# Kernel optimization log

Measured on AMD Instinct MI355X. Metric: run time of the kernel, lower is better.

Reference implementation:

```python
import jax, jax.numpy as jnp
import numpy as np

B, S, D, H, L, F = 1, 2048, 768, 12, 2, 3072
DH = D // H          # 64
W = 256              # one-sided sliding window (attention_window=512 total)
NC = S // W          # number of query chunks
VOCAB = 50265


def _ln(x, s, b, eps=1e-5):
    m = x.mean(-1, keepdims=True)
    v = ((x - m) ** 2).mean(-1, keepdims=True)
    return (x - m) / jnp.sqrt(v + eps) * s + b


def setup_inputs() -> dict:
    key = jax.random.key(0)
    ks = jax.random.split(key, 16)
    p = lambda k, sh: jax.random.normal(k, sh, jnp.float32) * 0.02
    return {
        "input_ids": jax.random.randint(ks[0], (B, S), 0, VOCAB),
        "attention_mask": jnp.ones((B, S), jnp.int32),
        "word_emb": p(ks[1], (VOCAB, D)),
        "pos_emb": p(ks[2], (S + 2, D)),          # roberta-style pos ids start at 2
        "type_emb": p(ks[3], (1, D)),
        "emb_ln_s": jnp.ones((D,), jnp.float32),
        "emb_ln_b": jnp.zeros((D,), jnp.float32),
        "Wqkv": p(ks[4], (L, 3, D, D)),
        "bqkv": jnp.zeros((L, 3, D), jnp.float32),
        "Wo": p(ks[5], (L, D, D)),
        "bo": jnp.zeros((L, D), jnp.float32),
        "ln1_s": jnp.ones((L, D), jnp.float32),
        "ln1_b": jnp.zeros((L, D), jnp.float32),
        "W1": p(ks[6], (L, D, F)),
        "b1": jnp.zeros((L, F), jnp.float32),
        "W2": p(ks[7], (L, F, D)),
        "b2": jnp.zeros((L, D), jnp.float32),
        "ln2_s": jnp.ones((L, D), jnp.float32),
        "ln2_b": jnp.zeros((L, D), jnp.float32),
        "pool_W": p(ks[8], (D, D)),
        "pool_b": jnp.zeros((D,), jnp.float32),
    }


def reference(input_ids, attention_mask, word_emb, pos_emb, type_emb,
              emb_ln_s, emb_ln_b, Wqkv, bqkv, Wo, bo, ln1_s, ln1_b,
              W1, b1, W2, b2, ln2_s, ln2_b, pool_W, pool_b):
    # ---- embeddings (roberta/longformer style) ----
    pos_ids = jnp.cumsum(attention_mask, axis=1) * attention_mask + 1  # padding_idx=1
    x = word_emb[input_ids] + pos_emb[pos_ids] + type_emb[0]
    x = _ln(x, emb_ln_s, emb_ln_b)

    # ---- banded-attention index/mask precompute (int constants) ----
    idx = jnp.arange(NC)[:, None] * W + jnp.arange(3 * W)[None, :]      # [NC, 3W] into padded seq
    rel = (jnp.arange(3 * W)[None, :] - W) - jnp.arange(W)[:, None]     # key_pos - query_pos
    band = (rel >= -W) & (rel <= W)                                      # [W, 3W]
    kmask = jnp.pad(attention_mask, ((0, 0), (W, W)))[:, idx].astype(bool)  # [B, NC, 3W]
    valid = band[None, None] & kmask[:, :, None, :]                      # [B, NC, W, 3W]

    inv_sqrt_dh = 1.0 / np.sqrt(DH)
    for l in range(L):
        qkv = jnp.einsum('bsd,tde->tbse', x, Wqkv[l]) + bqkv[l][:, None, None, :]
        q, k, v = [t.reshape(B, S, H, DH).transpose(0, 2, 1, 3) for t in qkv]  # [B,H,S,DH]
        qc = q.reshape(B, H, NC, W, DH)
        kp = jnp.pad(k, ((0, 0), (0, 0), (W, W), (0, 0)))
        vp = jnp.pad(v, ((0, 0), (0, 0), (W, W), (0, 0)))
        kc = kp[:, :, idx]                                               # [B,H,NC,3W,DH]
        vc = vp[:, :, idx]
        scores = jnp.einsum('bhcqd,bhckd->bhcqk', qc, kc) * inv_sqrt_dh  # [B,H,NC,W,3W]
        scores = jnp.where(valid[:, None], scores, -1e9)
        attn = jax.nn.softmax(scores, axis=-1)
        ctx = jnp.einsum('bhcqk,bhckd->bhcqd', attn, vc)
        ctx = ctx.reshape(B, H, S, DH).transpose(0, 2, 1, 3).reshape(B, S, D)
        x = _ln(x + ctx @ Wo[l] + bo[l], ln1_s[l], ln1_b[l])
        h = jax.nn.gelu(x @ W1[l] + b1[l], approximate=False)
        x = _ln(x + h @ W2[l] + b2[l], ln2_s[l], ln2_b[l])

    pooled = jnp.tanh(x[:, 0] @ pool_W + pool_b)
    return x, pooled
```

## Files before the change

### kernel.cpp

```cpp
#include <hip/hip_runtime.h>
#include <hip/hip_bf16.h>
#include <math.h>
#include <stddef.h>
#include <stdint.h>

typedef __hip_bfloat16 bf16;
typedef short bf16x8 __attribute__((ext_vector_type(8)));
typedef float f32x4 __attribute__((ext_vector_type(4)));

#define CS 2048
#define CD 768
#define CH 12
#define CDH 64
#define CF 3072
#define CW 256
#define CL 2
#define QKVN 2304
#define SDC ((size_t)CS * CD)

__device__ __forceinline__ void gload_lds16(const bf16* g, bf16* l) {
  __builtin_amdgcn_global_load_lds(
      (const __attribute__((address_space(1))) void*)g,
      (__attribute__((address_space(3))) void*)l, 16, 0, 0);
}

__device__ __forceinline__ float block_reduce_sum(float v, float* buf) {
  #pragma unroll
  for (int off = 32; off > 0; off >>= 1) v += __shfl_down(v, off, 64);
  int wid = threadIdx.x >> 6;
  __syncthreads();
  if ((threadIdx.x & 63) == 0) buf[wid] = v;
  __syncthreads();
  if (threadIdx.x == 0) buf[0] = buf[0] + buf[1] + buf[2] + buf[3];
  __syncthreads();
  return buf[0];
}

__global__ __launch_bounds__(256) void scan_kernel(const int* __restrict__ mask,
                                                   int* __restrict__ pos) {
  __shared__ int part[256];
  int tid = threadIdx.x;
  int mv[8]; int s = 0;
  #pragma unroll
  for (int i = 0; i < 8; ++i) { mv[i] = mask[tid * 8 + i]; s += mv[i]; }
  part[tid] = s;
  __syncthreads();
  for (int off = 1; off < 256; off <<= 1) {
    int t = 0;
    if (tid >= off) t = part[tid - off];
    __syncthreads();
    part[tid] += t;
    __syncthreads();
  }
  int run = part[tid] - s;
  #pragma unroll
  for (int i = 0; i < 8; ++i) {
    run += mv[i];
    pos[tid * 8 + i] = run * mv[i] + 1;
  }
}

__global__ __launch_bounds__(256) void transpose_conv(
    const float* __restrict__ in, bf16* __restrict__ out, int K, int N) {
  __shared__ float tile[32][33];
  int bn = blockIdx.x * 32, bk = blockIdx.y * 32;
  const float* src = in + (size_t)blockIdx.z * K * N;
  bf16* dst = out + (size_t)blockIdx.z * K * N;
  int tx = threadIdx.x, ty = threadIdx.y;
  #pragma unroll
  for (int i = 0; i < 32; i += 8)
    tile[ty + i][tx] = src[(size_t)(bk + ty + i) * N + bn + tx];
  __syncthreads();
  #pragma unroll
  for (int i = 0; i < 32; i += 8)
    dst[(size_t)(bn + ty + i) * K + bk + tx] = __float2bfloat16(tile[tx][ty + i]);
}

__global__ __launch_bounds__(256) void embed_ln_kernel(
    const int* __restrict__ ids, const int* __restrict__ pos,
    const float* __restrict__ wemb, const float* __restrict__ pemb,
    const float* __restrict__ temb, const float* __restrict__ gs,
    const float* __restrict__ gb, float* __restrict__ x, bf16* __restrict__ xb) {
  __shared__ float red[4];
  int srow = blockIdx.x;
  long long id = ids[srow];
  long long pid = pos[srow];
  float v[3];
  #pragma unroll
  for (int i = 0; i < 3; ++i) {
    int d = threadIdx.x + i * 256;
    v[i] = wemb[id * CD + d] + pemb[pid * CD + d] + temb[d];
  }
  float sum = v[0] + v[1] + v[2];
  sum = block_reduce_sum(sum, red);
  float mean = sum * (1.0f / CD);
  float sq = 0.f;
  #pragma unroll
  for (int i = 0; i < 3; ++i) { float c = v[i] - mean; sq += c * c; }
  sq = block_reduce_sum(sq, red);
  float rstd = rsqrtf(sq * (1.0f / CD) + 1e-5f);
  #pragma unroll
  for (int i = 0; i < 3; ++i) {
    int d = threadIdx.x + i * 256;
    float o = (v[i] - mean) * rstd * gs[d] + gb[d];
    x[(size_t)srow * CD + d] = o;
    xb[(size_t)srow * CD + d] = __float2bfloat16(o);
  }
}

template<int GELU, int OUTBF16, int SPLITS>
__global__ __launch_bounds__(256) void gemm_mfma(
    const bf16* __restrict__ A, const bf16* __restrict__ Bt,
    const float* __restrict__ bias, void* __restrict__ Cout,
    int M, int N, int Ktot) {
  __shared__ __align__(16) bf16 As[128 * 32];
  __shared__ __align__(16) bf16 Bs[128 * 32];
  const int tid = threadIdx.x;
  const int wave = tid >> 6, lane = tid & 63;
  const int m0 = blockIdx.y * 128, n0 = blockIdx.x * 128;
  const int wm = (wave & 1) * 64, wn = (wave >> 1) * 64;
  const int quad = lane >> 4, rsel = lane & 15;
  const int r_in = lane >> 2;
  const int chunk = lane & 3;
  const int Klen = Ktot / SPLITS;
  const int koff = (SPLITS > 1) ? blockIdx.z * Klen : 0;

  f32x4 acc[4][4] = {};

  for (int k0 = 0; k0 < Klen; k0 += 32) {
    #pragma unroll
    for (int i = 0; i < 4; ++i) {
      int op = wave * 4 + i;
      if (op < 8) {
        int row = op * 16 + r_in;
        gload_lds16(A + (size_t)(m0 + row) * Ktot + koff + k0 + chunk * 8, &As[op * 512]);
      } else {
        int row = (op - 8) * 16 + r_in;
        gload_lds16(Bt + (size_t)(n0 + row) * Ktot + koff + k0 + chunk * 8, &Bs[(op - 8) * 512]);
      }
    }
    __syncthreads();
    bf16x8 af[4], bfr[4];
    #pragma unroll
    for (int i = 0; i < 4; ++i)
      af[i] = *(const bf16x8*)&As[(wm + i * 16 + rsel) * 32 + quad * 8];
    #pragma unroll
    for (int j = 0; j < 4; ++j)
      bfr[j] = *(const bf16x8*)&Bs[(wn + j * 16 + rsel) * 32 + quad * 8];
    #pragma unroll
    for (int i = 0; i < 4; ++i)
      #pragma unroll
      for (int j = 0; j < 4; ++j)
        acc[i][j] = __builtin_amdgcn_mfma_f32_16x16x32_bf16(af[i], bfr[j], acc[i][j], 0, 0, 0);
    __syncthreads();
  }
  #pragma unroll
  for (int j = 0; j < 4; ++j) {
    int col = n0 + wn + j * 16 + rsel;
    float bv = (SPLITS == 1 || blockIdx.z == 0) ? bias[col] : 0.f;
    #pragma unroll
    for (int i = 0; i < 4; ++i) {
      #pragma unroll
      for (int r = 0; r < 4; ++r) {
        int rowm = m0 + wm + i * 16 + quad * 4 + r;
        float v = acc[i][j][r] + bv;
        if (GELU) v = 0.5f * v * (1.0f + erff(v * 0.70710678118654752f));
        if (OUTBF16) ((bf16*)Cout)[(size_t)rowm * N + col] = __float2bfloat16(v);
        else ((float*)Cout)[(size_t)blockIdx.z * M * N + (size_t)rowm * N + col] = v;
      }
    }
  }
}

__global__ __launch_bounds__(256) void vtrans_kernel(
    const bf16* __restrict__ qkv, bf16* __restrict__ vT) {
  __shared__ bf16 t[64][72];
  int s0 = blockIdx.x * 64, h = blockIdx.y;
  int r = threadIdx.x >> 2, cc = (threadIdx.x & 3) * 16;
  const bf16* src = qkv + (size_t)(s0 + r) * QKVN + 1536 + h * CDH + cc;
  *(bf16x8*)&t[r][cc] = *(const bf16x8*)src;
  *(bf16x8*)&t[r][cc + 8] = *(const bf16x8*)(src + 8);
  __syncthreads();
  int dh = threadIdx.x >> 2, sc = (threadIdx.x & 3) * 16;
  bf16 tmp[16];
  #pragma unroll
  for (int j = 0; j < 16; ++j) tmp[j] = t[sc + j][dh];
  bf16* dst = vT + (size_t)(h * CDH + dh) * CS + s0 + sc;
  *(bf16x8*)dst = *(bf16x8*)&tmp[0];
  *(bf16x8*)(dst + 8) = *(bf16x8*)&tmp[8];
}

__global__ __launch_bounds__(256) void attn_mfma(
    const bf16* __restrict__ qkv, const bf16* __restrict__ vT,
    const int* __restrict__ mask, bf16* __restrict__ ctx) {
  __shared__ bf16 Ps[4][16][72];
  const int h = blockIdx.y;
  const int q0 = blockIdx.x * 64;
  const int tid = threadIdx.x;
  const int wv = tid >> 6, lane = tid & 63;
  const int quad = lane >> 4, rsel = lane & 15;
  const int qw = q0 + wv * 16;

  const bf16* qp = &qkv[(size_t)(qw + rsel) * QKVN + h * CDH + quad * 8];
  bf16x8 qf0 = *(const bf16x8*)qp;
  bf16x8 qf1 = *(const bf16x8*)(qp + 32);

  float mi[4], li[4];
  f32x4 o[4] = {};
  #pragma unroll
  for (int r = 0; r < 4; ++r) { mi[r] = -1e30f; li[r] = 0.f; }

  #pragma unroll 1
  for (int kt = 0; kt < 9; ++kt) {
    int kbase = qw - CW + kt * 64;
    if (kbase + 63 < 0 || kbase >= CS) continue;

    f32x4 sc[4];
    #pragma unroll
    for (int nt = 0; nt < 4; ++nt) {
      int pp = kbase + nt * 16 + rsel;
      int ppc = min(max(pp, 0), CS - 1);
      const bf16* kp = &qkv[(size_t)ppc * QKVN + 768 + h * CDH + quad * 8];
      bf16x8 kf0 = *(const bf16x8*)kp;
      bf16x8 kf1 = *(const bf16x8*)(kp + 32);
      f32x4 z = {};
      z = __builtin_amdgcn_mfma_f32_16x16x32_bf16(qf0, kf0, z, 0, 0, 0);
      z = __builtin_amdgcn_mfma_f32_16x16x32_bf16(qf1, kf1, z, 0, 0, 0);
      sc[nt] = z;
    }
    float mx[4] = {-1e30f, -1e30f, -1e30f, -1e30f};
    #pragma unroll
    for (int nt = 0; nt < 4; ++nt) {
      int pp = kbase + nt * 16 + rsel;
      int ppc = min(max(pp, 0), CS - 1);
      bool kvld = (pp >= 0) && (pp < CS) && (mask[ppc] != 0);
      #pragma unroll
      for (int r = 0; r < 4; ++r) {
        int qr = qw + quad * 4 + r;
        float s = sc[nt][r] * 0.125f;
        bool band = (pp >= qr - CW) && (pp <= qr + CW);
        s = (kvld && band) ? s : -1e9f;
        sc[nt][r] = s;
        mx[r] = fmaxf(mx[r], s);
      }
    }
    #pragma unroll
    for (int r = 0; r < 4; ++r) {
      #pragma unroll
      for (int off = 1; off < 16; off <<= 1)
        mx[r] = fmaxf(mx[r], __shfl_xor(mx[r], off, 64));
    }
    float al[4], rs[4] = {};
    #pragma unroll
    for (int r = 0; r < 4; ++r) {
      float mn = fmaxf(mi[r], mx[r]);
      al[r] = __expf(mi[r] - mn);
      mi[r] = mn;
    }
    #pragma unroll
    for (int nt = 0; nt < 4; ++nt)
      #pragma unroll
      for (int r = 0; r < 4; ++r) {
        float p = __expf(sc[nt][r] - mi[r]);
        sc[nt][r] = p;
        rs[r] += p;
      }
    #pragma unroll
    for (int r = 0; r < 4; ++r) {
      #pragma unroll
      for (int off = 1; off < 16; off <<= 1)
        rs[r] += __shfl_xor(rs[r], off, 64);
      li[r] = li[r] * al[r] + rs[r];
    }
    #pragma unroll
    for (int d = 0; d < 4; ++d)
      #pragma unroll
      for (int r = 0; r < 4; ++r) o[d][r] *= al[r];
    #pragma unroll
    for (int nt = 0; nt < 4; ++nt)
      #pragma unroll
      for (int r = 0; r < 4; ++r)
        Ps[wv][quad * 4 + r][nt * 16 + rsel] = __float2bfloat16(sc[nt][r]);
    __asm__ volatile("s_waitcnt lgkmcnt(0)" ::: "memory");
    bf16x8 pf0 = *(const bf16x8*)&Ps[wv][rsel][quad * 8];
    bf16x8 pf1 = *(const bf16x8*)&Ps[wv][rsel][32 + quad * 8];
    int kc0 = min(max(kbase + quad * 8, 0), CS - 8);
    int kc1 = min(max(kbase + 32 + quad * 8, 0), CS - 8);
    #pragma unroll
    for (int d = 0; d < 4; ++d) {
      const bf16* vrow = &vT[(size_t)(h * CDH + d * 16 + rsel) * CS];
      bf16x8 vf0 = *(const bf16x8*)(vrow + kc0);
      bf16x8 vf1 = *(const bf16x8*)(vrow + kc1);
      o[d] = __builtin_amdgcn_mfma_f32_16x16x32_bf16(pf0, vf0, o[d], 0, 0, 0);
      o[d] = __builtin_amdgcn_mfma_f32_16x16x32_bf16(pf1, vf1, o[d], 0, 0, 0);
    }
  }
  float inv[4];
  #pragma unroll
  for (int r = 0; r < 4; ++r) inv[r] = 1.0f / li[r];
  #pragma unroll
  for (int d = 0; d < 4; ++d)
    #pragma unroll
    for (int r = 0; r < 4; ++r)
      ctx[(size_t)(qw + quad * 4 + r) * CD + h * CDH + d * 16 + rsel] =
          __float2bfloat16(o[d][r] * inv[r]);
}

template<int P>
__global__ __launch_bounds__(256) void add_ln_kernel(
    const float* __restrict__ g, const float* __restrict__ xin,
    float* __restrict__ xout, bf16* __restrict__ xb,
    const float* __restrict__ gs, const float* __restrict__ gb) {
  __shared__ float red[4];
  int srow = blockIdx.x;
  float v[3];
  #pragma unroll
  for (int i = 0; i < 3; ++i) {
    int d = threadIdx.x + i * 256;
    size_t idx = (size_t)srow * CD + d;
    float a = xin[idx];
    #pragma unroll
    for (int p = 0; p < P; ++p) a += g[p * SDC + idx];
    v[i] = a;
  }
  float sum = v[0] + v[1] + v[2];
  sum = block_reduce_sum(sum, red);
  float mean = sum * (1.0f / CD);
  float sq = 0.f;
  #pragma unroll
  for (int i = 0; i < 3; ++i) { float c = v[i] - mean; sq += c * c; }
  sq = block_reduce_sum(sq, red);
  float rstd = rsqrtf(sq * (1.0f / CD) + 1e-5f);
  #pragma unroll
  for (int i = 0; i < 3; ++i) {
    int d = threadIdx.x + i * 256;
    float o = (v[i] - mean) * rstd * gs[d] + gb[d];
    xout[(size_t)srow * CD + d] = o;
    xb[(size_t)srow * CD + d] = __float2bfloat16(o);
  }
}

__global__ __launch_bounds__(256) void pool_kernel(
    const float* __restrict__ x, const float* __restrict__ Wp,
    const float* __restrict__ bp, float* __restrict__ out) {
  __shared__ float xs[CD];
  __shared__ float red[4][64];
  int t = threadIdx.x;
  for (int i = t; i < CD; i += 256) xs[i] = x[i];
  __syncthreads();
  int n = blockIdx.x * 64 + (t & 63);
  int kp = t >> 6;
  float acc = 0.f;
  #pragma unroll 4
  for (int kk = kp * 192; kk < kp * 192 + 192; ++kk)
    acc = fmaf(xs[kk], Wp[(size_t)kk * CD + n], acc);
  red[kp][t & 63] = acc;
  __syncthreads();
  if (t < 64) {
    int nn = blockIdx.x * 64 + t;
    out[nn] = tanhf(red[0][t] + red[1][t] + red[2][t] + red[3][t] + bp[nn]);
  }
}

extern "C" void kernel_launch(void* const* d_in, const int* in_sizes, int n_in,
                              void* d_out, int out_size, void* d_ws, size_t ws_size,
                              hipStream_t stream) {
  const int*   ids   = (const int*)d_in[0];
  const int*   mask  = (const int*)d_in[1];
  const float* wemb  = (const float*)d_in[2];
  const float* pemb  = (const float*)d_in[3];
  const float* temb  = (const float*)d_in[4];
  const float* elns  = (const float*)d_in[5];
  const float* elnb  = (const float*)d_in[6];
  const float* Wqkv  = (const float*)d_in[7];
  const float* bqkv  = (const float*)d_in[8];
  const float* Wo    = (const float*)d_in[9];
  const float* bo    = (const float*)d_in[10];
  const float* ln1s  = (const float*)d_in[11];
  const float* ln1b  = (const float*)d_in[12];
  const float* W1    = (const float*)d_in[13];
  const float* b1    = (const float*)d_in[14];
  const float* W2    = (const float*)d_in[15];
  const float* b2    = (const float*)d_in[16];
  const float* ln2s  = (const float*)d_in[17];
  const float* ln2b  = (const float*)d_in[18];
  const float* poolW = (const float*)d_in[19];
  const float* poolb = (const float*)d_in[20];

  const size_t SD = SDC;
  const size_t SF = (size_t)CS * CF;

  char* w = (char*)d_ws;
  float* x    = (float*)w; w += SD * 4;
  bf16*  xb   = (bf16*)w;  w += SD * 2;
  bf16*  qkv  = (bf16*)w;  w += (size_t)CS * QKVN * 2;
  bf16*  vT   = (bf16*)w;  w += SD * 2;
  bf16*  ctxb = (bf16*)w;  w += SD * 2;
  bf16*  t1b  = (bf16*)w;  w += SF * 2;
  float* t2   = (float*)w; w += SD * 4 * 4;
  int*   pos  = (int*)w;   w += (size_t)CS * 4;
  bf16* WqkvT = (bf16*)w;  w += (size_t)CL * QKVN * CD * 2;
  bf16* WoT   = (bf16*)w;  w += (size_t)CL * CD * CD * 2;
  bf16* W1T   = (bf16*)w;  w += (size_t)CL * CF * CD * 2;
  bf16* W2T   = (bf16*)w;  w += (size_t)CL * CD * CF * 2;

  dim3 tb(32, 8);
  scan_kernel<<<1, 256, 0, stream>>>(mask, pos);
  transpose_conv<<<dim3(CD/32, CD/32, CL*3), tb, 0, stream>>>(Wqkv, WqkvT, CD, CD);
  transpose_conv<<<dim3(CD/32, CD/32, CL),   tb, 0, stream>>>(Wo,   WoT,   CD, CD);
  transpose_conv<<<dim3(CF/32, CD/32, CL),   tb, 0, stream>>>(W1,   W1T,   CD, CF);
  transpose_conv<<<dim3(CD/32, CF/32, CL),   tb, 0, stream>>>(W2,   W2T,   CF, CD);
  embed_ln_kernel<<<CS, 256, 0, stream>>>(ids, pos, wemb, pemb, temb, elns, elnb, x, xb);

  for (int l = 0; l < CL; ++l) {
    gemm_mfma<0,1,1><<<dim3(QKVN/128, CS/128), 256, 0, stream>>>(
        xb, WqkvT + (size_t)l * QKVN * CD, bqkv + (size_t)l * 3 * CD, qkv, CS, QKVN, CD);
    vtrans_kernel<<<dim3(CS/64, CH), 256, 0, stream>>>(qkv, vT);
    attn_mfma<<<dim3(CS/64, CH), 256, 0, stream>>>(qkv, vT, mask, ctxb);
    gemm_mfma<0,0,2><<<dim3(CD/128, CS/128, 2), 256, 0, stream>>>(
        ctxb, WoT + (size_t)l * CD * CD, bo + (size_t)l * CD, t2, CS, CD, CD);
    add_ln_kernel<2><<<CS, 256, 0, stream>>>(t2, x, x, xb,
        ln1s + (size_t)l * CD, ln1b + (size_t)l * CD);
    gemm_mfma<1,1,1><<<dim3(CF/128, CS/128), 256, 0, stream>>>(
        xb, W1T + (size_t)l * CF * CD, b1 + (size_t)l * CF, t1b, CS, CF, CD);
    gemm_mfma<0,0,4><<<dim3(CD/128, CS/128, 4), 256, 0, stream>>>(
        t1b, W2T + (size_t)l * CD * CF, b2 + (size_t)l * CD, t2, CS, CD, CF);
    float* lastx = (l == CL - 1) ? (float*)d_out : x;
    add_ln_kernel<4><<<CS, 256, 0, stream>>>(t2, x, lastx, xb,
        ln2s + (size_t)l * CD, ln2b + (size_t)l * CD);
  }

  pool_kernel<<<12, 256, 0, stream>>>((float*)d_out, poolW, poolb, (float*)d_out + SD);
}
```

Before: 617.0 us.

## Fuse V transpose into QKV GEMM, split attention keys across waves, merge weight transposes

Three separate changes. The QKV GEMM epilogue now writes V columns straight into the transposed vT buffer, so the standalone vtrans kernel and its extra pass over V are gone. Attention blocks grow to 512 threads: two wave halves each cover part of the key tiles and their partial softmax states are combined through shared memory, which adds parallelism at the cost of more LDS and a block-wide barrier. The four weight transpose launches are folded into one kernel launch to cut launch overhead.

```diff
diff --git a/kernel.cpp b/kernel.cpp
--- a/kernel.cpp
+++ b/kernel.cpp
@@ -24,6 +24,11 @@
       (__attribute__((address_space(3))) void*)l, 16, 0, 0);
 }
 
+__device__ __forceinline__ unsigned short f2bu(float v) {
+  bf16 b = __float2bfloat16(v);
+  return *(unsigned short*)&b;
+}
+
 __device__ __forceinline__ float block_reduce_sum(float v, float* buf) {
   #pragma unroll
   for (int off = 32; off > 0; off >>= 1) v += __shfl_down(v, off, 64);
@@ -60,13 +65,30 @@
   }
 }
 
-__global__ __launch_bounds__(256) void transpose_conv(
-    const float* __restrict__ in, bf16* __restrict__ out, int K, int N) {
+__global__ __launch_bounds__(256) void transpose_all(
+    const float* __restrict__ Wqkv, const float* __restrict__ Wo,
+    const float* __restrict__ W1, const float* __restrict__ W2,
+    bf16* __restrict__ WqkvT, bf16* __restrict__ WoT,
+    bf16* __restrict__ W1T, bf16* __restrict__ W2T) {
   __shared__ float tile[32][33];
-  int bn = blockIdx.x * 32, bk = blockIdx.y * 32;
-  const float* src = in + (size_t)blockIdx.z * K * N;
-  bf16* dst = out + (size_t)blockIdx.z * K * N;
-  int tx = threadIdx.x, ty = threadIdx.y;
+  int b = blockIdx.x;
+  const float* src; bf16* dst; int K, N, t;
+  if (b < 3456) {
+    int mat = b / 576; t = b % 576; K = 768; N = 768;
+    src = Wqkv + (size_t)mat * 768 * 768; dst = WqkvT + (size_t)mat * 768 * 768;
+  } else if (b < 4608) {
+    b -= 3456; int mat = b / 576; t = b % 576; K = 768; N = 768;
+    src = Wo + (size_t)mat * 768 * 768; dst = WoT + (size_t)mat * 768 * 768;
+  } else if (b < 9216) {
+    b -= 4608; int mat = b / 2304; t = b % 2304; K = 768; N = 3072;
+    src = W1 + (size_t)mat * 768 * 3072; dst = W1T + (size_t)mat * 768 * 3072;
+  } else {
+    b -= 9216; int mat = b / 2304; t = b % 2304; K = 3072; N = 768;
+    src = W2 + (size_t)mat * 3072 * 768; dst = W2T + (size_t)mat * 3072 * 768;
+  }
+  int nt = N / 32;
+  int bn = (t % nt) * 32, bk = (t / nt) * 32;
+  int tx = threadIdx.x & 31, ty = (threadIdx.x >> 5) & 7;
   #pragma unroll
   for (int i = 0; i < 32; i += 8)
     tile[ty + i][tx] = src[(size_t)(bk + ty + i) * N + bn + tx];
@@ -108,11 +130,11 @@
   }
 }
 
-template<int GELU, int OUTBF16, int SPLITS>
+template<int GELU, int OUTBF16, int SPLITS, int VTFUSE>
 __global__ __launch_bounds__(256) void gemm_mfma(
     const bf16* __restrict__ A, const bf16* __restrict__ Bt,
     const float* __restrict__ bias, void* __restrict__ Cout,
-    int M, int N, int Ktot) {
+    bf16* __restrict__ vTout, int M, int N, int Ktot) {
   __shared__ __align__(16) bf16 As[128 * 32];
   __shared__ __align__(16) bf16 Bs[128 * 32];
   const int tid = threadIdx.x;
@@ -158,48 +180,47 @@
   for (int j = 0; j < 4; ++j) {
     int col = n0 + wn + j * 16 + rsel;
     float bv = (SPLITS == 1 || blockIdx.z == 0) ? bias[col] : 0.f;
-    #pragma unroll
-    for (int i = 0; i < 4; ++i) {
-      #pragma unroll
-      for (int r = 0; r < 4; ++r) {
-        int rowm = m0 + wm + i * 16 + quad * 4 + r;
-        float v = acc[i][j][r] + bv;
-        if (GELU) v = 0.5f * v * (1.0f + erff(v * 0.70710678118654752f));
-        if (OUTBF16) ((bf16*)Cout)[(size_t)rowm * N + col] = __float2bfloat16(v);
-        else ((float*)Cout)[(size_t)blockIdx.z * M * N + (size_t)rowm * N + col] = v;
-      }
-    }
-  }
-}
-
-__global__ __launch_bounds__(256) void vtrans_kernel(
-    const bf16* __restrict__ qkv, bf16* __restrict__ vT) {
-  __shared__ bf16 t[64][72];
-  int s0 = blockIdx.x * 64, h = blockIdx.y;
-  int r = threadIdx.x >> 2, cc = (threadIdx.x & 3) * 16;
-  const bf16* src = qkv + (size_t)(s0 + r) * QKVN + 1536 + h * CDH + cc;
-  *(bf16x8*)&t[r][cc] = *(const bf16x8*)src;
-  *(bf16x8*)&t[r][cc + 8] = *(const bf16x8*)(src + 8);
-  __syncthreads();
-  int dh = threadIdx.x >> 2, sc = (threadIdx.x & 3) * 16;
-  bf16 tmp[16];
-  #pragma unroll
-  for (int j = 0; j < 16; ++j) tmp[j] = t[sc + j][dh];
-  bf16* dst = vT + (size_t)(h * CDH + dh) * CS + s0 + sc;
-  *(bf16x8*)dst = *(bf16x8*)&tmp[0];
-  *(bf16x8*)(dst + 8) = *(bf16x8*)&tmp[8];
-}
-
-__global__ __launch_bounds__(256) void attn_mfma(
+    if (VTFUSE && col >= 1536) {
+      #pragma unroll
+      for (int i = 0; i < 4; ++i) {
+        int rowb = m0 + wm + i * 16 + quad * 4;
+        ushort4 pk;
+        pk.x = f2bu(acc[i][j][0] + bv);
+        pk.y = f2bu(acc[i][j][1] + bv);
+        pk.z = f2bu(acc[i][j][2] + bv);
+        pk.w = f2bu(acc[i][j][3] + bv);
+        *(ushort4*)&vTout[(size_t)(col - 1536) * CS + rowb] = pk;
+      }
+    } else {
+      #pragma unroll
+      for (int i = 0; i < 4; ++i) {
+        #pragma unroll
+        for (int r = 0; r < 4; ++r) {
+          int rowm = m0 + wm + i * 16 + quad * 4 + r;
+          float v = acc[i][j][r] + bv;
+          if (GELU) v = 0.5f * v * (1.0f + erff(v * 0.70710678118654752f));
+          if (OUTBF16) ((bf16*)Cout)[(size_t)rowm * N + col] = __float2bfloat16(v);
+          else ((float*)Cout)[(size_t)blockIdx.z * M * N + (size_t)rowm * N + col] = v;
+        }
+      }
+    }
+  }
+}
+
+__global__ __launch_bounds__(512) void attn_mfma(
     const bf16* __restrict__ qkv, const bf16* __restrict__ vT,
     const int* __restrict__ mask, bf16* __restrict__ ctx) {
-  __shared__ bf16 Ps[4][16][72];
+  __shared__ bf16 Ps[8][16][72];
+  __shared__ float Obuf[4][16][64];
+  __shared__ float Mbuf[4][16];
+  __shared__ float Lbuf[4][16];
   const int h = blockIdx.y;
   const int q0 = blockIdx.x * 64;
   const int tid = threadIdx.x;
   const int wv = tid >> 6, lane = tid & 63;
+  const int qg = wv & 3, half = wv >> 2;
   const int quad = lane >> 4, rsel = lane & 15;
-  const int qw = q0 + wv * 16;
+  const int qw = q0 + qg * 16;
 
   const bf16* qp = &qkv[(size_t)(qw + rsel) * QKVN + h * CDH + quad * 8];
   bf16x8 qf0 = *(const bf16x8*)qp;
@@ -210,8 +231,9 @@
   #pragma unroll
   for (int r = 0; r < 4; ++r) { mi[r] = -1e30f; li[r] = 0.f; }
 
+  const int kt0 = half ? 5 : 0, kt1 = half ? 9 : 5;
   #pragma unroll 1
-  for (int kt = 0; kt < 9; ++kt) {
+  for (int kt = kt0; kt < kt1; ++kt) {
     int kbase = qw - CW + kt * 64;
     if (kbase + 63 < 0 || kbase >= CS) continue;
 
@@ -295,15 +317,38 @@
       o[d] = __builtin_amdgcn_mfma_f32_16x16x32_bf16(pf1, vf1, o[d], 0, 0, 0);
     }
   }
-  float inv[4];
-  #pragma unroll
-  for (int r = 0; r < 4; ++r) inv[r] = 1.0f / li[r];
-  #pragma unroll
-  for (int d = 0; d < 4; ++d)
-    #pragma unroll
-    for (int r = 0; r < 4; ++r)
-      ctx[(size_t)(qw + quad * 4 + r) * CD + h * CDH + d * 16 + rsel] =
-          __float2bfloat16(o[d][r] * inv[r]);
+
+  if (half == 1) {
+    #pragma unroll
+    for (int d = 0; d < 4; ++d)
+      #pragma unroll
+      for (int r = 0; r < 4; ++r)
+        Obuf[qg][quad * 4 + r][d * 16 + rsel] = o[d][r];
+    if (rsel == 0) {
+      #pragma unroll
+      for (int r = 0; r < 4; ++r) {
+        Mbuf[qg][quad * 4 + r] = mi[r];
+        Lbuf[qg][quad * 4 + r] = li[r];
+      }
+    }
+  }
+  __syncthreads();
+  if (half == 0) {
+    #pragma unroll
+    for (int r = 0; r < 4; ++r) {
+      int row = quad * 4 + r;
+      float m1 = Mbuf[qg][row], l1 = Lbuf[qg][row];
+      float mn = fmaxf(mi[r], m1);
+      float a0 = __expf(mi[r] - mn);
+      float a1 = __expf(m1 - mn);
+      float inv = 1.0f / (li[r] * a0 + l1 * a1);
+      #pragma unroll
+      for (int d = 0; d < 4; ++d) {
+        float val = (o[d][r] * a0 + Obuf[qg][row][d * 16 + rsel] * a1) * inv;
+        ctx[(size_t)(qw + row) * CD + h * CDH + d * 16 + rsel] = __float2bfloat16(val);
+      }
+    }
+  }
 }
 
 template<int P>
@@ -404,27 +449,22 @@
   bf16* W1T   = (bf16*)w;  w += (size_t)CL * CF * CD * 2;
   bf16* W2T   = (bf16*)w;  w += (size_t)CL * CD * CF * 2;
 
-  dim3 tb(32, 8);
   scan_kernel<<<1, 256, 0, stream>>>(mask, pos);
-  transpose_conv<<<dim3(CD/32, CD/32, CL*3), tb, 0, stream>>>(Wqkv, WqkvT, CD, CD);
-  transpose_conv<<<dim3(CD/32, CD/32, CL),   tb, 0, stream>>>(Wo,   WoT,   CD, CD);
-  transpose_conv<<<dim3(CF/32, CD/32, CL),   tb, 0, stream>>>(W1,   W1T,   CD, CF);
-  transpose_conv<<<dim3(CD/32, CF/32, CL),   tb, 0, stream>>>(W2,   W2T,   CF, CD);
+  transpose_all<<<13824, 256, 0, stream>>>(Wqkv, Wo, W1, W2, WqkvT, WoT, W1T, W2T);
   embed_ln_kernel<<<CS, 256, 0, stream>>>(ids, pos, wemb, pemb, temb, elns, elnb, x, xb);
 
   for (int l = 0; l < CL; ++l) {
-    gemm_mfma<0,1,1><<<dim3(QKVN/128, CS/128), 256, 0, stream>>>(
-        xb, WqkvT + (size_t)l * QKVN * CD, bqkv + (size_t)l * 3 * CD, qkv, CS, QKVN, CD);
-    vtrans_kernel<<<dim3(CS/64, CH), 256, 0, stream>>>(qkv, vT);
-    attn_mfma<<<dim3(CS/64, CH), 256, 0, stream>>>(qkv, vT, mask, ctxb);
-    gemm_mfma<0,0,2><<<dim3(CD/128, CS/128, 2), 256, 0, stream>>>(
-        ctxb, WoT + (size_t)l * CD * CD, bo + (size_t)l * CD, t2, CS, CD, CD);
+    gemm_mfma<0,1,1,1><<<dim3(QKVN/128, CS/128), 256, 0, stream>>>(
+        xb, WqkvT + (size_t)l * QKVN * CD, bqkv + (size_t)l * 3 * CD, qkv, vT, CS, QKVN, CD);
+    attn_mfma<<<dim3(CS/64, CH), 512, 0, stream>>>(qkv, vT, mask, ctxb);
+    gemm_mfma<0,0,2,0><<<dim3(CD/128, CS/128, 2), 256, 0, stream>>>(
+        ctxb, WoT + (size_t)l * CD * CD, bo + (size_t)l * CD, t2, nullptr, CS, CD, CD);
     add_ln_kernel<2><<<CS, 256, 0, stream>>>(t2, x, x, xb,
         ln1s + (size_t)l * CD, ln1b + (size_t)l * CD);
-    gemm_mfma<1,1,1><<<dim3(CF/128, CS/128), 256, 0, stream>>>(
-        xb, W1T + (size_t)l * CF * CD, b1 + (size_t)l * CF, t1b, CS, CF, CD);
-    gemm_mfma<0,0,4><<<dim3(CD/128, CS/128, 4), 256, 0, stream>>>(
-        t1b, W2T + (size_t)l * CD * CF, b2 + (size_t)l * CD, t2, CS, CD, CF);
+    gemm_mfma<1,1,1,0><<<dim3(CF/128, CS/128), 256, 0, stream>>>(
+        xb, W1T + (size_t)l * CF * CD, b1 + (size_t)l * CF, t1b, nullptr, CS, CF, CD);
+    gemm_mfma<0,0,4,0><<<dim3(CD/128, CS/128, 4), 256, 0, stream>>>(
+        t1b, W2T + (size_t)l * CD * CF, b2 + (size_t)l * CD, t2, nullptr, CS, CD, CF);
     float* lastx = (l == CL - 1) ? (float*)d_out : x;
     add_ln_kernel<4><<<CS, 256, 0, stream>>>(t2, x, lastx, xb,
         ln2s + (size_t)l * CD, ln2b + (size_t)l * CD);
```

Result: faster. 598.7 us (-3.0%).
